# Optimization experiments

Measured on AMD Instinct MI355X. Metric: run time of the kernel, lower is better.

The kernel has to match this reference:

```python
import jax, jax.numpy as jnp
import numpy as np

HEADS = 4
DIM_HEAD = 32


def setup_inputs() -> dict:
    key = jax.random.key(0)
    k1, k2, k3, k4 = jax.random.split(key, 4)
    b, dim, t = 8, 64, 16384
    inner = HEADS * DIM_HEAD  # 128
    x = jax.random.normal(k1, (b, dim, t), dtype=jnp.float32)
    # Conv1d(dim, inner*3, kernel=1, bias=False) -> weight (3*inner, dim)
    w_qkv = jax.random.normal(k2, (3 * inner, dim), dtype=jnp.float32) * (1.0 / np.sqrt(dim))
    # Conv1d(inner, dim, kernel=1) -> weight (dim, inner), bias (dim,)
    w_out = jax.random.normal(k3, (dim, inner), dtype=jnp.float32) * (1.0 / np.sqrt(inner))
    b_out = jax.random.normal(k4, (dim,), dtype=jnp.float32) * 0.01
    return {"x": x, "w_qkv": w_qkv, "w_out": w_out, "b_out": b_out}


def reference(x, w_qkv, w_out, b_out):
    b, c, t = x.shape
    h, dh = HEADS, DIM_HEAD
    # 1x1 conv == per-timestep matmul: (b, 3*inner, t)
    qkv = jnp.einsum('oc,bct->bot', w_qkv, x)
    q, k, v = jnp.split(qkv, 3, axis=1)
    q = q.reshape(b, h, dh, t)
    k = k.reshape(b, h, dh, t)
    v = v.reshape(b, h, dh, t)
    q = jax.nn.softmax(q, axis=-1)   # softmax over time
    k = jax.nn.softmax(k, axis=-2)   # softmax over head-dim d
    # einsum('bhdt,bhds->bhds', k, v): sums k over t, broadcast-scales v
    context = jnp.einsum('bhdt,bhds->bhds', k, v)
    # einsum('bhdt,bhds->bhdt', q, context): sums context over s, scales q
    out = jnp.einsum('bhdt,bhds->bhdt', q, context)
    out = out.reshape(b, h * dh, t)
    # to_out 1x1 conv with bias
    return jnp.einsum('oc,bct->bot', w_out, out) + b_out[None, :, None]
```

## Files before the change

kernel.cpp:

```cpp
#include <hip/hip_runtime.h>
#include <math.h>


typedef short short8 __attribute__((ext_vector_type(8)));
typedef short short4s __attribute__((ext_vector_type(4)));
typedef float f32x4 __attribute__((ext_vector_type(4)));

namespace {
constexpr int NB = 8;
constexpr int NC = 64;
constexpr int NT = 16384;
constexpr int NI = 128;
constexpr int TBK = 256;
constexpr int CPB = NT / TBK;
constexpr int NBLK = NB * CPB;
constexpr int XSP = 72;
constexpr int PTP = 136;
constexpr int PT  = 32;

constexpr int F_ZQ = 0;
constexpr int F_KS = NI;
constexpr int F_XS = 2 * NI;
constexpr int SLOT = 2 * NI + NC;
constexpr int WS_NFLOAT = NB * CPB * SLOT;
constexpr size_t P_ELEMS = (size_t)NB * NT * NI;
constexpr size_t WS_BYTES_NEEDED = (size_t)WS_NFLOAT * 4 + P_ELEMS * 2;
}

__device__ __forceinline__ unsigned short f2bf(float f) {
  unsigned u = __float_as_uint(f);
  u += 0x7fffu + ((u >> 16) & 1u);
  return (unsigned short)(u >> 16);
}

__device__ __forceinline__ void stage_x(const float* __restrict__ xb, int t0,
                                        unsigned short* xs, float* xsum_dst, int tid) {
  const int c = tid >> 2, tq = tid & 3;
  const float4* xr = (const float4*)(xb + (size_t)c * NT + t0);
  float s = 0.f;
#pragma unroll 4
  for (int i = 0; i < TBK / 16; ++i) {
    const int tv = tq + 4 * i;
    float4 v = xr[tv];
    s += (v.x + v.y) + (v.z + v.w);
    const int t = 4 * tv;
    xs[(t + 0) * XSP + c] = f2bf(v.x);
    xs[(t + 1) * XSP + c] = f2bf(v.y);
    xs[(t + 2) * XSP + c] = f2bf(v.z);
    xs[(t + 3) * XSP + c] = f2bf(v.w);
  }
  s += __shfl_xor(s, 1, 64);
  s += __shfl_xor(s, 2, 64);
  if (tq == 0) xsum_dst[c] = s;
}

__device__ __forceinline__ void load_aq(const float* __restrict__ wqkv, int w,
                                        int lm, int quad, short8 aq[2][2]) {
#pragma unroll
  for (int tile = 0; tile < 2; ++tile)
#pragma unroll
    for (int s = 0; s < 2; ++s) {
      const float* pq = wqkv + (size_t)(32 * w + tile * 16 + lm) * NC + s * 32 + quad * 8;
#pragma unroll
      for (int j = 0; j < 8; ++j) aq[tile][s][j] = (short)f2bf(pq[j]);
    }
}

__global__ __launch_bounds__(256) void la_stats(
    const float* __restrict__ x, const float* __restrict__ wqkv,
    float* __restrict__ ws)
{
  __shared__ __align__(16) unsigned short xs[TBK * XSP];

  const int bid = blockIdx.x;
  const int b = bid >> 6, chunk = bid & 63;
  const int tid = threadIdx.x, lane = tid & 63;
  const int w = __builtin_amdgcn_readfirstlane(tid >> 6);
  const int lm = lane & 15, quad = lane >> 4;
  const float* xb = x + (size_t)b * NC * NT;
  float* slot = ws + (size_t)(b * CPB + chunk) * SLOT;
  unsigned short* Pb = (unsigned short*)(ws + WS_NFLOAT)
                       + (size_t)(b * CPB + chunk) * TBK * NI;

  stage_x(xb, chunk * TBK, xs, slot + F_XS, tid);

  short8 aq[2][2], ak[2][2];
  load_aq(wqkv, w, lm, quad, aq);
#pragma unroll
  for (int tile = 0; tile < 2; ++tile)
#pragma unroll
    for (int s = 0; s < 2; ++s) {
      const float* pk = wqkv + (size_t)(NI + 32 * w + tile * 16 + lm) * NC + s * 32 + quad * 8;
#pragma unroll
      for (int j = 0; j < 8; ++j) ak[tile][s][j] = (short)f2bf(pk[j]);
    }

  float zq_acc[2][4] = {};
  float ks_acc[2][4] = {};
  __syncthreads();

  for (int tc = 0; tc < TBK / 16; ++tc) {
    short8 bf[2];
#pragma unroll
    for (int s = 0; s < 2; ++s)
      bf[s] = *(const short8*)&xs[(tc * 16 + lm) * XSP + s * 32 + quad * 8];
    f32x4 cq[2] = {{0,0,0,0},{0,0,0,0}}, ck[2] = {{0,0,0,0},{0,0,0,0}};
#pragma unroll
    for (int tile = 0; tile < 2; ++tile)
#pragma unroll
      for (int s = 0; s < 2; ++s) {
        cq[tile] = __builtin_amdgcn_mfma_f32_16x16x32_bf16(aq[tile][s], bf[s], cq[tile], 0, 0, 0);
        ck[tile] = __builtin_amdgcn_mfma_f32_16x16x32_bf16(ak[tile][s], bf[s], ck[tile], 0, 0, 0);
      }
    float ke[2][4];
    float zt = 0.f;
#pragma unroll
    for (int tile = 0; tile < 2; ++tile) {
      short4s pv;
#pragma unroll
      for (int r = 0; r < 4; ++r) {
        float eq = __expf(cq[tile][r]);
        zq_acc[tile][r] += eq;
        pv[r] = (short)f2bf(eq);
        float e = __expf(ck[tile][r]);
        ke[tile][r] = e;
        zt += e;
      }
      *(short4s*)&Pb[(size_t)(tc * 16 + lm) * NI + 32 * w + tile * 16 + quad * 4] = pv;
    }
    zt += __shfl_xor(zt, 16, 64);
    zt += __shfl_xor(zt, 32, 64);
    const float rz = __builtin_amdgcn_rcpf(zt);
#pragma unroll
    for (int tile = 0; tile < 2; ++tile)
#pragma unroll
      for (int r = 0; r < 4; ++r)
        ks_acc[tile][r] = fmaf(ke[tile][r], rz, ks_acc[tile][r]);
  }

#pragma unroll
  for (int tile = 0; tile < 2; ++tile)
#pragma unroll
    for (int r = 0; r < 4; ++r) {
      float a = zq_acc[tile][r], k = ks_acc[tile][r];
#pragma unroll
      for (int off = 1; off < 16; off <<= 1) {
        a += __shfl_xor(a, off, 64);
        k += __shfl_xor(k, off, 64);
      }
      if (lm == 0) {
        const int c = 32 * w + tile * 16 + quad * 4 + r;
        slot[F_ZQ + c] = a;
        slot[F_KS + c] = k;
      }
    }
}

__global__ __launch_bounds__(256) void la_gemm(
    const float* __restrict__ wqkv, const float* __restrict__ wout,
    const float* __restrict__ bout, const float* __restrict__ ws,
    float* __restrict__ y)
{
  __shared__ __align__(16) unsigned short ptile[PT * PTP];
  __shared__ float scale_s[NI];
  __shared__ float xsum_s[NC];

  const int bid = blockIdx.x;
  const int b = bid >> 6, chunk = bid & 63;
  const int tid = threadIdx.x, lane = tid & 63;
  const int w = __builtin_amdgcn_readfirstlane(tid >> 6);
  const int lm = lane & 15, quad = lane >> 4;
  const int t0 = chunk * TBK;
  const float* wsb = ws + (size_t)b * CPB * SLOT;
  const unsigned short* Pb = (const unsigned short*)(ws + WS_NFLOAT)
                             + (size_t)(b * CPB + chunk) * TBK * NI;

  if (tid < NC) {
    float s = 0.f;
#pragma unroll 8
    for (int sl = 0; sl < CPB; ++sl) s += wsb[(size_t)sl * SLOT + F_XS + tid];
    xsum_s[tid] = s;
  }
  __syncthreads();
  if (tid < NI) {
    float vs = 0.f;
    const float* wv = wqkv + (size_t)(2 * NI + tid) * NC;
#pragma unroll 8
    for (int cc = 0; cc < NC; ++cc) vs = fmaf(wv[cc], xsum_s[cc], vs);
    float zq_t = 0.f, ks_t = 0.f;
#pragma unroll 8
    for (int sl = 0; sl < CPB; ++sl) {
      zq_t += wsb[(size_t)sl * SLOT + F_ZQ + tid];
      ks_t += wsb[(size_t)sl * SLOT + F_KS + tid];
    }
    scale_s[tid] = ks_t * vs / zq_t;
  }
  __syncthreads();

  short8 aw[4];
  {
    const int o = 16 * w + lm;
#pragma unroll
    for (int s = 0; s < 4; ++s) {
      const float* wo = wout + (size_t)o * NI + s * 32 + quad * 8;
#pragma unroll
      for (int j = 0; j < 8; ++j)
        aw[s][j] = (short)f2bf(wo[j] * scale_s[s * 32 + quad * 8 + j]);
    }
  }
  float bias[4];
#pragma unroll
  for (int r = 0; r < 4; ++r) bias[r] = bout[16 * w + quad * 4 + r];

  const int tl0 = tid >> 4;
  const int coff = (tid & 15) * 8;
  for (int sub = 0; sub < TBK / PT; ++sub) {
#pragma unroll
    for (int i = 0; i < 2; ++i) {
      const int tl = i * 16 + tl0;
      short8 v = *(const short8*)&Pb[(size_t)(sub * PT + tl) * NI + coff];
      *(short8*)&ptile[tl * PTP + coff] = v;
    }
    __syncthreads();
    for (int tc = 0; tc < PT / 16; ++tc) {
      short8 bp[4];
#pragma unroll
      for (int s = 0; s < 4; ++s)
        bp[s] = *(const short8*)&ptile[(tc * 16 + lm) * PTP + s * 32 + quad * 8];
      f32x4 acc = {bias[0], bias[1], bias[2], bias[3]};
#pragma unroll
      for (int s = 0; s < 4; ++s)
        acc = __builtin_amdgcn_mfma_f32_16x16x32_bf16(aw[s], bp[s], acc, 0, 0, 0);
#pragma unroll
      for (int r = 0; r < 4; ++r)
        y[((size_t)b * NC + 16 * w + quad * 4 + r) * NT + t0 + sub * PT + tc * 16 + lm] = acc[r];
    }
    __syncthreads();
  }
}

extern "C" void kernel_launch(void* const* d_in, const int* in_sizes, int n_in,
                              void* d_out, int out_size, void* d_ws, size_t ws_size,
                              hipStream_t stream)
{
  const float* x    = (const float*)d_in[0];
  const float* wqkv = (const float*)d_in[1];
  const float* wout = (const float*)d_in[2];
  const float* bout = (const float*)d_in[3];
  float* y  = (float*)d_out;
  float* ws = (float*)d_ws;

  if (ws_size < WS_BYTES_NEEDED) return;

  la_stats<<<dim3(NBLK), 256, 0, stream>>>(x, wqkv, ws);
  la_gemm<<<dim3(NBLK), 256, 0, stream>>>(wqkv, wout, bout, ws, y);
}
```

Baseline: 117.6 us.

## Double-buffer x and P tiles in LDS to overlap loads with MFMA

In the stats kernel, x is now staged in 64-timestep quarters into two LDS buffers, so the next quarter loads while MFMA and exp work runs on the current one. The x-sum is accumulated across quarters. In the gemm kernel, the P tile is also double-buffered and one of the two barriers per step is dropped. The goal is to hide global-load latency behind compute, and the stats kernel also uses much less LDS, which may allow more blocks per CU. The cost is more barriers in the stats kernel and a software prefetch that only overlaps if the compiler keeps the loads in flight.

```diff
diff --git a/kernel.cpp b/kernel.cpp
--- a/kernel.cpp
+++ b/kernel.cpp
@@ -14,6 +14,8 @@
 constexpr int TBK = 256;
 constexpr int CPB = NT / TBK;
 constexpr int NBLK = NB * CPB;
+constexpr int QT  = 64;
+constexpr int NQ  = TBK / QT;
 constexpr int XSP = 72;
 constexpr int PTP = 136;
 constexpr int PT  = 32;
@@ -33,27 +35,6 @@
   return (unsigned short)(u >> 16);
 }
 
-__device__ __forceinline__ void stage_x(const float* __restrict__ xb, int t0,
-                                        unsigned short* xs, float* xsum_dst, int tid) {
-  const int c = tid >> 2, tq = tid & 3;
-  const float4* xr = (const float4*)(xb + (size_t)c * NT + t0);
-  float s = 0.f;
-#pragma unroll 4
-  for (int i = 0; i < TBK / 16; ++i) {
-    const int tv = tq + 4 * i;
-    float4 v = xr[tv];
-    s += (v.x + v.y) + (v.z + v.w);
-    const int t = 4 * tv;
-    xs[(t + 0) * XSP + c] = f2bf(v.x);
-    xs[(t + 1) * XSP + c] = f2bf(v.y);
-    xs[(t + 2) * XSP + c] = f2bf(v.z);
-    xs[(t + 3) * XSP + c] = f2bf(v.w);
-  }
-  s += __shfl_xor(s, 1, 64);
-  s += __shfl_xor(s, 2, 64);
-  if (tq == 0) xsum_dst[c] = s;
-}
-
 __device__ __forceinline__ void load_aq(const float* __restrict__ wqkv, int w,
                                         int lm, int quad, short8 aq[2][2]) {
 #pragma unroll
@@ -70,7 +51,7 @@
     const float* __restrict__ x, const float* __restrict__ wqkv,
     float* __restrict__ ws)
 {
-  __shared__ __align__(16) unsigned short xs[TBK * XSP];
+  __shared__ __align__(16) unsigned short xs[2][QT * XSP];
 
   const int bid = blockIdx.x;
   const int b = bid >> 6, chunk = bid & 63;
@@ -82,7 +63,9 @@
   unsigned short* Pb = (unsigned short*)(ws + WS_NFLOAT)
                        + (size_t)(b * CPB + chunk) * TBK * NI;
 
-  stage_x(xb, chunk * TBK, xs, slot + F_XS, tid);
+  const int sc = tid >> 2, tq = tid & 3;
+  const float4* xr = (const float4*)(xb + (size_t)sc * NT + chunk * TBK);
+  float xsum_partial = 0.f;
 
   short8 aq[2][2], ak[2][2];
   load_aq(wqkv, w, lm, quad, aq);
@@ -95,47 +78,75 @@
       for (int j = 0; j < 8; ++j) ak[tile][s][j] = (short)f2bf(pk[j]);
     }
 
+  auto stage_q = [&](int h) {
+    unsigned short* xd = xs[h & 1];
+#pragma unroll
+    for (int i = 0; i < 4; ++i) {
+      const int tv = tq + 4 * i;
+      float4 v = xr[h * (QT / 4) + tv];
+      xsum_partial += (v.x + v.y) + (v.z + v.w);
+      const int t = 4 * tv;
+      xd[(t + 0) * XSP + sc] = f2bf(v.x);
+      xd[(t + 1) * XSP + sc] = f2bf(v.y);
+      xd[(t + 2) * XSP + sc] = f2bf(v.z);
+      xd[(t + 3) * XSP + sc] = f2bf(v.w);
+    }
+  };
+
   float zq_acc[2][4] = {};
   float ks_acc[2][4] = {};
-  __syncthreads();
-
-  for (int tc = 0; tc < TBK / 16; ++tc) {
-    short8 bf[2];
-#pragma unroll
-    for (int s = 0; s < 2; ++s)
-      bf[s] = *(const short8*)&xs[(tc * 16 + lm) * XSP + s * 32 + quad * 8];
-    f32x4 cq[2] = {{0,0,0,0},{0,0,0,0}}, ck[2] = {{0,0,0,0},{0,0,0,0}};
-#pragma unroll
-    for (int tile = 0; tile < 2; ++tile)
-#pragma unroll
-      for (int s = 0; s < 2; ++s) {
-        cq[tile] = __builtin_amdgcn_mfma_f32_16x16x32_bf16(aq[tile][s], bf[s], cq[tile], 0, 0, 0);
-        ck[tile] = __builtin_amdgcn_mfma_f32_16x16x32_bf16(ak[tile][s], bf[s], ck[tile], 0, 0, 0);
+
+  stage_q(0);
+  for (int h = 0; h < NQ; ++h) {
+    __syncthreads();
+    if (h + 1 < NQ) stage_q(h + 1);
+    const unsigned short* xsrc = xs[h & 1];
+
+    for (int tc = 0; tc < QT / 16; ++tc) {
+      short8 bf[2];
+#pragma unroll
+      for (int s = 0; s < 2; ++s)
+        bf[s] = *(const short8*)&xsrc[(tc * 16 + lm) * XSP + s * 32 + quad * 8];
+      f32x4 cq[2] = {{0,0,0,0},{0,0,0,0}}, ck[2] = {{0,0,0,0},{0,0,0,0}};
+#pragma unroll
+      for (int tile = 0; tile < 2; ++tile)
+#pragma unroll
+        for (int s = 0; s < 2; ++s) {
+          cq[tile] = __builtin_amdgcn_mfma_f32_16x16x32_bf16(aq[tile][s], bf[s], cq[tile], 0, 0, 0);
+          ck[tile] = __builtin_amdgcn_mfma_f32_16x16x32_bf16(ak[tile][s], bf[s], ck[tile], 0, 0, 0);
+        }
+      float ke[2][4];
+      float zt = 0.f;
+#pragma unroll
+      for (int tile = 0; tile < 2; ++tile) {
+        short4s pv;
+#pragma unroll
+        for (int r = 0; r < 4; ++r) {
+          float eq = __expf(cq[tile][r]);
+          zq_acc[tile][r] += eq;
+          pv[r] = (short)f2bf(eq);
+          float e = __expf(ck[tile][r]);
+          ke[tile][r] = e;
+          zt += e;
+        }
+        *(short4s*)&Pb[(size_t)(h * QT + tc * 16 + lm) * NI + 32 * w + tile * 16 + quad * 4] = pv;
       }
-    float ke[2][4];
-    float zt = 0.f;
-#pragma unroll
-    for (int tile = 0; tile < 2; ++tile) {
-      short4s pv;
-#pragma unroll
-      for (int r = 0; r < 4; ++r) {
-        float eq = __expf(cq[tile][r]);
-        zq_acc[tile][r] += eq;
-        pv[r] = (short)f2bf(eq);
-        float e = __expf(ck[tile][r]);
-        ke[tile][r] = e;
-        zt += e;
-      }
-      *(short4s*)&Pb[(size_t)(tc * 16 + lm) * NI + 32 * w + tile * 16 + quad * 4] = pv;
-    }
-    zt += __shfl_xor(zt, 16, 64);
-    zt += __shfl_xor(zt, 32, 64);
-    const float rz = __builtin_amdgcn_rcpf(zt);
-#pragma unroll
-    for (int tile = 0; tile < 2; ++tile)
-#pragma unroll
-      for (int r = 0; r < 4; ++r)
-        ks_acc[tile][r] = fmaf(ke[tile][r], rz, ks_acc[tile][r]);
+      zt += __shfl_xor(zt, 16, 64);
+      zt += __shfl_xor(zt, 32, 64);
+      const float rz = __builtin_amdgcn_rcpf(zt);
+#pragma unroll
+      for (int tile = 0; tile < 2; ++tile)
+#pragma unroll
+        for (int r = 0; r < 4; ++r)
+          ks_acc[tile][r] = fmaf(ke[tile][r], rz, ks_acc[tile][r]);
+    }
+  }
+
+  {
+    float s = xsum_partial;
+    s += __shfl_xor(s, 1, 64);
+    s += __shfl_xor(s, 2, 64);
+    if (tq == 0) slot[F_XS + sc] = s;
   }
 
 #pragma unroll
@@ -161,7 +172,7 @@
     const float* __restrict__ bout, const float* __restrict__ ws,
     float* __restrict__ y)
 {
-  __shared__ __align__(16) unsigned short ptile[PT * PTP];
+  __shared__ __align__(16) unsigned short ptile[2][PT * PTP];
   __shared__ float scale_s[NI];
   __shared__ float xsum_s[NC];
 
@@ -214,19 +225,27 @@
 
   const int tl0 = tid >> 4;
   const int coff = (tid & 15) * 8;
-  for (int sub = 0; sub < TBK / PT; ++sub) {
+
+  auto stage_p = [&](int sub) {
+    unsigned short* pd = ptile[sub & 1];
 #pragma unroll
     for (int i = 0; i < 2; ++i) {
       const int tl = i * 16 + tl0;
       short8 v = *(const short8*)&Pb[(size_t)(sub * PT + tl) * NI + coff];
-      *(short8*)&ptile[tl * PTP + coff] = v;
-    }
+      *(short8*)&pd[tl * PTP + coff] = v;
+    }
+  };
+
+  stage_p(0);
+  for (int sub = 0; sub < TBK / PT; ++sub) {
     __syncthreads();
+    if (sub + 1 < TBK / PT) stage_p(sub + 1);
+    const unsigned short* psrc = ptile[sub & 1];
     for (int tc = 0; tc < PT / 16; ++tc) {
       short8 bp[4];
 #pragma unroll
       for (int s = 0; s < 4; ++s)
-        bp[s] = *(const short8*)&ptile[(tc * 16 + lm) * PTP + s * 32 + quad * 8];
+        bp[s] = *(const short8*)&psrc[(tc * 16 + lm) * PTP + s * 32 + quad * 8];
       f32x4 acc = {bias[0], bias[1], bias[2], bias[3]};
 #pragma unroll
       for (int s = 0; s < 4; ++s)
@@ -235,7 +254,6 @@
       for (int r = 0; r < 4; ++r)
         y[((size_t)b * NC + 16 * w + quad * 4 + r) * NT + t0 + sub * PT + tc * 16 + lm] = acc[r];
     }
-    __syncthreads();
   }
 }
 
```

Result: no change. 119.7 us (+1.8%).
